# Performance work log

Measured on AMD Instinct MI355X. Metric: run time of the kernel, lower is better.

Reference implementation:

```python
import jax, jax.numpy as jnp
import numpy as np

N, L = 32, 2048
C_S, C_E, C_H, K, NRES = 384, 32, 128, 7, 20
C_IN = C_S + C_E  # 416
EPS = 1e-8


def setup_inputs() -> dict:
    key = jax.random.key(0)
    ks = jax.random.split(key, 32)
    s = 0.02
    d = {}
    d['aa_seq'] = jax.random.randint(ks[0], (L,), 0, NRES)
    d['sfea_tns'] = jax.random.normal(ks[1], (N, L, C_S), jnp.float32)
    d['sfea_tns_init'] = jax.random.normal(ks[2], (N, L, C_S), jnp.float32)
    d['encd_tns'] = jax.random.normal(ks[3], (N, L, C_E), jnp.float32)
    d['quat_tns'] = jax.random.normal(ks[4], (N, L, 4), jnp.float32)
    d['trsl_tns'] = jax.random.normal(ks[5], (N, L, 3), jnp.float32)
    # FrameHead linears
    d['Wq'] = jax.random.normal(ks[6], (C_IN, 4), jnp.float32) * s
    d['bq'] = jnp.zeros((4,), jnp.float32)
    d['Wt'] = jax.random.normal(ks[7], (C_IN, 3), jnp.float32) * s
    d['bt'] = jnp.zeros((3,), jnp.float32)
    # 20 per-residue-type AngleHead experts, stacked on leading axis
    d['Wa1'] = jax.random.normal(ks[8], (NRES, C_IN, C_H), jnp.float32) * s
    d['ba1'] = jnp.zeros((NRES, C_H), jnp.float32)
    d['Wa2'] = jax.random.normal(ks[9], (NRES, C_IN, C_H), jnp.float32) * s
    d['ba2'] = jnp.zeros((NRES, C_H), jnp.float32)
    d['Wb1a'] = jax.random.normal(ks[10], (NRES, C_H, C_H), jnp.float32) * s
    d['bb1a'] = jnp.zeros((NRES, C_H), jnp.float32)
    d['Wb1b'] = jax.random.normal(ks[11], (NRES, C_H, C_H), jnp.float32) * s
    d['bb1b'] = jnp.zeros((NRES, C_H), jnp.float32)
    d['Wb2a'] = jax.random.normal(ks[12], (NRES, C_H, C_H), jnp.float32) * s
    d['bb2a'] = jnp.zeros((NRES, C_H), jnp.float32)
    d['Wb2b'] = jax.random.normal(ks[13], (NRES, C_H, C_H), jnp.float32) * s
    d['bb2b'] = jnp.zeros((NRES, C_H), jnp.float32)
    d['Wout'] = jax.random.normal(ks[14], (NRES, C_H, K * 2), jnp.float32) * s
    d['bout'] = jnp.zeros((NRES, K * 2), jnp.float32)
    return d


def _qnorm(q):
    return q * jax.lax.rsqrt(jnp.sum(q * q, -1, keepdims=True) + EPS)


def _quat_mul(q, p):
    w1, x1, y1, z1 = jnp.split(q, 4, -1)
    w2, x2, y2, z2 = jnp.split(p, 4, -1)
    return jnp.concatenate([
        w1 * w2 - x1 * x2 - y1 * y2 - z1 * z2,
        w1 * x2 + x1 * w2 + y1 * z2 - z1 * y2,
        w1 * y2 - x1 * z2 + y1 * w2 + z1 * x2,
        w1 * z2 + x1 * y2 - y1 * x2 + z1 * w2], -1)


def _quat_rotate(q, v):
    # rotate vector v by unit quaternion q = (w, xyz)
    w, qv = q[..., :1], q[..., 1:]
    t = 2.0 * jnp.cross(qv, v)
    return v + w * t + jnp.cross(qv, t)


def _angle_net(sfcd, sfcd_init, aa, Wa1, ba1, Wa2, ba2,
               Wb1a, bb1a, Wb1b, bb1b, Wb2a, bb2a, Wb2b, bb2b, Wout, bout):
    # residue-type routed AngleHead: gather each token's expert weights by aa index
    g = lambda W: jnp.take(W, aa, axis=0)  # [L, ...]
    relu = jax.nn.relu
    a = (jnp.einsum('nlc,lch->nlh', relu(sfcd), g(Wa1)) + g(ba1)
         + jnp.einsum('nlc,lch->nlh', relu(sfcd_init), g(Wa2)) + g(ba2))
    # residual block 1
    h = jnp.einsum('nlh,lhk->nlk', relu(a), g(Wb1a)) + g(bb1a)
    a = a + jnp.einsum('nlh,lhk->nlk', relu(h), g(Wb1b)) + g(bb1b)
    # residual block 2
    h = jnp.einsum('nlh,lhk->nlk', relu(a), g(Wb2a)) + g(bb2a)
    a = a + jnp.einsum('nlh,lhk->nlk', relu(h), g(Wb2b)) + g(bb2b)
    out = jnp.einsum('nlh,lhk->nlk', relu(a), g(Wout)) + g(bout)  # [N,L,2K]
    ang = out.reshape(out.shape[0], out.shape[1], K, 2)
    norm = jnp.sqrt(jnp.sum(ang * ang, -1, keepdims=True) + 1e-12)
    return ang / norm


def reference(aa_seq, sfea_tns, sfea_tns_init, encd_tns, quat_tns, trsl_tns,
              Wq, bq, Wt, bt, Wa1, ba1, Wa2, ba2, Wb1a, bb1a, Wb1b, bb1b,
              Wb2a, bb2a, Wb2b, bb2b, Wout, bout):
    sfcd = jnp.concatenate([sfea_tns, encd_tns], -1)          # [N,L,C_IN]
    sfcd_init = jnp.concatenate([sfea_tns_init, encd_tns], -1)
    # FrameHead: quaternion/translation update signals
    quat_upd = sfcd @ Wq + bq                                  # [N,L,4]
    trsl_upd = sfcd @ Wt + bt                                  # [N,L,3]
    q_old = _qnorm(quat_tns)
    quat_new = _qnorm(_quat_mul(q_old, _qnorm(quat_upd)))
    trsl_new = trsl_tns + _quat_rotate(q_old, trsl_upd)
    angl_tns = _angle_net(sfcd, sfcd_init, aa_seq, Wa1, ba1, Wa2, ba2,
                          Wb1a, bb1a, Wb1b, bb1b, Wb2a, bb2a, Wb2b, bb2b,
                          Wout, bout)
    return quat_new, trsl_new, angl_tns, quat_upd
```

## Files before the change

kernel.cpp:

```cpp
#include <hip/hip_runtime.h>

#define L_SEQ 2048
#define CS 384
#define CE 32
#define CIN 416
#define CH 128
#define NRES 20

#define ABST 136
#define PADN 2068
#define NB2  1034

#define PERM_REGION 4608
#define WA_PER (CH*CIN)
#define WB_PER (CH*CH)
#define WO_PER (16*CH)
#define OFF_WA1T 0
#define OFF_WA2T (NRES*WA_PER)
#define OFF_WB1AT (2*NRES*WA_PER)
#define OFF_WB1BT (OFF_WB1AT + 1*NRES*WB_PER)
#define OFF_WB2AT (OFF_WB1AT + 2*NRES*WB_PER)
#define OFF_WB2BT (OFF_WB1AT + 3*NRES*WB_PER)
#define OFF_WOUTT (OFF_WB1AT + 4*NRES*WB_PER)
#define TOTW (OFF_WOUTT + NRES*WO_PER)

#define OUT_TR 262144
#define OUT_ANG 458752
#define OUT_QU 1376256

#define LOSCALE 4096.0f
#define ILOSCALE (1.0f/4096.0f)
#define F16MIN 6.1035156e-5f

typedef _Float16 f16x8 __attribute__((ext_vector_type(8)));
typedef _Float16 f16x4 __attribute__((ext_vector_type(4)));
typedef float f32x4 __attribute__((ext_vector_type(4)));

#define MFMA16 __builtin_amdgcn_mfma_f32_16x16x32_f16

static __device__ __forceinline__ void split1(float x, _Float16& h, _Float16& l) {
  _Float16 hi = (__builtin_fabsf(x) < F16MIN) ? (_Float16)0.f : (_Float16)x;
  h = hi;
  l = (_Float16)((x - (float)hi) * LOSCALE);
}

__global__ __launch_bounds__(256) void quat_head(
    const float* __restrict__ sfea, const float* __restrict__ encd,
    const float* __restrict__ quat, const float* __restrict__ trsl,
    const float* __restrict__ Wq, const float* __restrict__ bq,
    const float* __restrict__ Wt, const float* __restrict__ bt,
    float* __restrict__ out) {
  const int wv   = threadIdx.x >> 6;
  const int lane = threadIdx.x & 63;
  const size_t idx = (size_t)blockIdx.x * 4 + wv;
  const float* __restrict__ srow = sfea + idx * CS;

  float q0=0,q1=0,q2=0,q3=0,t0=0,t1=0,t2=0;
  #pragma unroll
  for (int cc = 0; cc < 6; ++cc) {
    const int ch = cc*64 + lane;
    const float s = srow[ch];
    const float4 wq = *reinterpret_cast<const float4*>(Wq + (size_t)ch*4);
    const float* wt = Wt + (size_t)ch*3;
    q0 += s*wq.x; q1 += s*wq.y; q2 += s*wq.z; q3 += s*wq.w;
    t0 += s*wt[0]; t1 += s*wt[1]; t2 += s*wt[2];
  }
  if (lane < CE) {
    const float s = encd[idx*CE + lane];
    const int ch = CS + lane;
    const float4 wq = *reinterpret_cast<const float4*>(Wq + (size_t)ch*4);
    const float* wt = Wt + (size_t)ch*3;
    q0 += s*wq.x; q1 += s*wq.y; q2 += s*wq.z; q3 += s*wq.w;
    t0 += s*wt[0]; t1 += s*wt[1]; t2 += s*wt[2];
  }
  #pragma unroll
  for (int off = 1; off < 64; off <<= 1) {
    q0 += __shfl_xor(q0, off); q1 += __shfl_xor(q1, off);
    q2 += __shfl_xor(q2, off); q3 += __shfl_xor(q3, off);
    t0 += __shfl_xor(t0, off); t1 += __shfl_xor(t1, off);
    t2 += __shfl_xor(t2, off);
  }
  if (lane == 0) {
    const float u0 = q0 + bq[0], u1 = q1 + bq[1], u2 = q2 + bq[2], u3 = q3 + bq[3];
    const float v0 = t0 + bt[0], v1 = t1 + bt[1], v2 = t2 + bt[2];
    float a0 = quat[idx*4+0], a1 = quat[idx*4+1], a2 = quat[idx*4+2], a3 = quat[idx*4+3];
    const float rq = rsqrtf(a0*a0+a1*a1+a2*a2+a3*a3 + 1e-8f);
    a0*=rq; a1*=rq; a2*=rq; a3*=rq;
    const float ru = rsqrtf(u0*u0+u1*u1+u2*u2+u3*u3 + 1e-8f);
    const float p0=u0*ru, p1=u1*ru, p2=u2*ru, p3=u3*ru;
    const float mw = a0*p0 - a1*p1 - a2*p2 - a3*p3;
    const float mx = a0*p1 + a1*p0 + a2*p3 - a3*p2;
    const float my = a0*p2 - a1*p3 + a2*p0 + a3*p1;
    const float mz = a0*p3 + a1*p2 - a2*p1 + a3*p0;
    const float rm = rsqrtf(mw*mw+mx*mx+my*my+mz*mz + 1e-8f);
    out[idx*4+0]=mw*rm; out[idx*4+1]=mx*rm; out[idx*4+2]=my*rm; out[idx*4+3]=mz*rm;
    const float tx = 2.f*(a2*v2 - a3*v1);
    const float ty = 2.f*(a3*v0 - a1*v2);
    const float tz = 2.f*(a1*v1 - a2*v0);
    out[OUT_TR + idx*3+0] = trsl[idx*3+0] + v0 + a0*tx + (a2*tz - a3*ty);
    out[OUT_TR + idx*3+1] = trsl[idx*3+1] + v1 + a0*ty + (a3*tx - a1*tz);
    out[OUT_TR + idx*3+2] = trsl[idx*3+2] + v2 + a0*tz + (a1*ty - a2*tx);
    out[OUT_QU + idx*4+0]=u0; out[OUT_QU + idx*4+1]=u1;
    out[OUT_QU + idx*4+2]=u2; out[OUT_QU + idx*4+3]=u3;
  }
}

__global__ __launch_bounds__(1024) void build_perm(const int* __restrict__ aa_seq,
                                                   unsigned short* __restrict__ perm) {
  __shared__ int cnt[NRES*32];
  __shared__ int woff[NRES*32];
  __shared__ int poff_s[NRES];
  __shared__ int ctot_s[NRES];
  const int t = threadIdx.x;
  const int wv = t >> 6, lane = t & 63;

  for (int i = t; i < PADN; i += 1024) perm[i] = 0;

  int aav[2];
  #pragma unroll
  for (int h = 0; h < 2; ++h) {
    const int W = wv + h*16;
    aav[h] = aa_seq[W*64 + lane];
    #pragma unroll
    for (int a = 0; a < NRES; ++a) {
      const unsigned long long m = __ballot(aav[h] == a);
      if (lane == a) cnt[a*32 + W] = (int)__popcll(m);
    }
  }
  __syncthreads();
  if (t < 32) {
    int tot = 0;
    if (t < NRES) {
      #pragma unroll
      for (int W = 0; W < 32; ++W) tot += cnt[t*32 + W];
    }
    const int pa = (t < NRES) ? ((tot + 1) & ~1) : 0;
    int s = pa;
    #pragma unroll
    for (int o = 1; o < 32; o <<= 1) {
      const int u = __shfl_up(s, o);
      if (lane >= o) s += u;
    }
    if (t < NRES) { poff_s[t] = s - pa; ctot_s[t] = tot; }
    for (int a = 0; a < NRES; ++a) {
      const int v0 = cnt[a*32 + t];
      int v = v0;
      #pragma unroll
      for (int o = 1; o < 32; o <<= 1) {
        const int u = __shfl_up(v, o);
        if (lane >= o) v += u;
      }
      woff[a*32 + t] = poff_s[a] + v - v0;
    }
  }
  __syncthreads();
  const unsigned long long ltmask = (lane == 0) ? 0ull : (~0ull >> (64 - lane));
  #pragma unroll
  for (int h = 0; h < 2; ++h) {
    const int W = wv + h*16;
    const int a = aav[h];
    int pos = 0;
    #pragma unroll
    for (int aq = 0; aq < NRES; ++aq) {
      const unsigned long long m = __ballot(a == aq);
      if (a == aq) pos = woff[aq*32 + W] + (int)__popcll(m & ltmask);
    }
    const unsigned short lv = (unsigned short)(W*64 + lane);
    perm[pos] = lv;
    if ((ctot_s[a] & 1) && pos == poff_s[a] + ctot_s[a] - 1) perm[pos + 1] = lv;
  }
}

__global__ __launch_bounds__(256) void convert_w(
    const float* __restrict__ Wa1, const float* __restrict__ Wa2,
    const float* __restrict__ Wb1a, const float* __restrict__ Wb1b,
    const float* __restrict__ Wb2a, const float* __restrict__ Wb2b,
    const float* __restrict__ Wout, _Float16* __restrict__ wsw) {
  const int idx = blockIdx.x * 256 + threadIdx.x;
  if (idx >= TOTW) return;
  float v;
  if (idx < OFF_WB1AT) {
    const int which = (idx < OFF_WA2T) ? 0 : 1;
    const float* W = which ? Wa2 : Wa1;
    int r = idx - which * OFF_WA2T;
    const int aa = r / WA_PER; r -= aa * WA_PER;
    const int h = r / CIN;     const int c = r - h * CIN;
    v = W[((size_t)aa*CIN + c)*CH + h];
  } else if (idx < OFF_WOUTT) {
    int q = idx - OFF_WB1AT;
    const int which = q / (NRES*WB_PER);
    int r = q - which * (NRES*WB_PER);
    const float* W = (which==0)?Wb1a:(which==1)?Wb1b:(which==2)?Wb2a:Wb2b;
    const int aa = r / WB_PER; r -= aa * WB_PER;
    const int h = r / CH;      const int c = r - h * CH;
    v = W[((size_t)aa*CH + c)*CH + h];
  } else {
    int r = idx - OFF_WOUTT;
    const int aa = r / WO_PER; r -= aa * WO_PER;
    const int kk = r / CH;     const int c = r - kk * CH;
    v = (kk < 14) ? Wout[((size_t)aa*CH + c)*14 + kk] : 0.f;
  }
  _Float16 h, l; split1(v, h, l);
  wsw[idx] = h;
  wsw[(size_t)TOTW + idx] = l;
}

static __device__ __forceinline__ void fold(f32x4 acc[2][2], const f32x4 accL[2][2],
                                            float b0, float b1) {
  #pragma unroll
  for (int m = 0; m < 2; ++m)
    #pragma unroll
    for (int i = 0; i < 4; ++i) {
      acc[m][0][i] += accL[m][0][i]*ILOSCALE + b0;
      acc[m][1][i] += accL[m][1][i]*ILOSCALE + b1;
    }
}

static __device__ __forceinline__ void store_relu_pair(_Float16* dh, _Float16* dl,
    const f32x4 acc[2][2], int lane, int h0) {
  const int lr = lane & 15;
  const int r0 = (lane >> 4) << 2;
  #pragma unroll
  for (int m = 0; m < 2; ++m)
    #pragma unroll
    for (int p = 0; p < 2; ++p)
      #pragma unroll
      for (int i = 0; i < 4; ++i) {
        const float v = fmaxf(acc[m][p][i], 0.f);
        _Float16 hh, ll; split1(v, hh, ll);
        const int idx = (m*16 + r0 + i)*ABST + h0 + p*16 + lr;
        dh[idx] = hh; dl[idx] = ll;
      }
}

template<int S>
static __device__ __forceinline__ void gemm_dual(
    const _Float16* aH0, const _Float16* aL0,
    const _Float16* aH1, const _Float16* aL1,
    const _Float16* __restrict__ wH,
    int kbase, int nks,
    f32x4 acc0[2][2], f32x4 acc0L[2][2],
    f32x4 acc1[2][2], f32x4 acc1L[2][2],
    int lane, int h0) {
  const int lr = lane & 15;
  const int lk = (lane >> 4) << 3;
  #pragma unroll
  for (int ks = 0; ks < nks; ++ks) {
    const int kl = ks*32 + lk;
    const int kg = kbase + kl;
    const _Float16* p0 = wH + (size_t)(h0+lr)*S + kg;
    const _Float16* p1 = wH + (size_t)(h0+16+lr)*S + kg;
    const f16x8 b0h = *(const f16x8*)p0;
    const f16x8 b0l = *(const f16x8*)(p0 + TOTW);
    const f16x8 b1h = *(const f16x8*)p1;
    const f16x8 b1l = *(const f16x8*)(p1 + TOTW);
#define DOPOS(AH, AL, AC, ACL) { \
    const f16x8 a0h = *(const f16x8*)(AH + lr*ABST + kl); \
    const f16x8 a0l = *(const f16x8*)(AL + lr*ABST + kl); \
    const f16x8 a1h = *(const f16x8*)(AH + (lr+16)*ABST + kl); \
    const f16x8 a1l = *(const f16x8*)(AL + (lr+16)*ABST + kl); \
    AC[0][0]  = MFMA16(a0h, b0h, AC[0][0], 0,0,0); \
    ACL[0][0] = MFMA16(a0h, b0l, ACL[0][0], 0,0,0); \
    ACL[0][0] = MFMA16(a0l, b0h, ACL[0][0], 0,0,0); \
    AC[1][0]  = MFMA16(a1h, b0h, AC[1][0], 0,0,0); \
    ACL[1][0] = MFMA16(a1h, b0l, ACL[1][0], 0,0,0); \
    ACL[1][0] = MFMA16(a1l, b0h, ACL[1][0], 0,0,0); \
    AC[0][1]  = MFMA16(a0h, b1h, AC[0][1], 0,0,0); \
    ACL[0][1] = MFMA16(a0h, b1l, ACL[0][1], 0,0,0); \
    ACL[0][1] = MFMA16(a0l, b1h, ACL[0][1], 0,0,0); \
    AC[1][1]  = MFMA16(a1h, b1h, AC[1][1], 0,0,0); \
    ACL[1][1] = MFMA16(a1h, b1l, ACL[1][1], 0,0,0); \
    ACL[1][1] = MFMA16(a1l, b1h, ACL[1][1], 0,0,0); }
    DOPOS(aH0, aL0, acc0, acc0L)
    DOPOS(aH1, aL1, acc1, acc1L)
#undef DOPOS
  }
}

static __device__ __forceinline__ void stage_row128(
    const float* __restrict__ row, _Float16* dH, _Float16* dL, int n, int sj) {
  #pragma unroll
  for (int q2 = 0; q2 < 2; ++q2) {
    const int cl = q2*64 + sj*8;
    const float4 v0 = *(const float4*)(row + cl);
    const float4 v1 = *(const float4*)(row + cl + 4);
    const float xs[8] = {v0.x,v0.y,v0.z,v0.w,v1.x,v1.y,v1.z,v1.w};
    f16x8 h8, l8;
    #pragma unroll
    for (int e = 0; e < 8; ++e) {
      _Float16 hh, ll; split1(fmaxf(xs[e], 0.f), hh, ll);
      h8[e] = hh; l8[e] = ll;
    }
    *(f16x8*)(dH + n*ABST + cl) = h8;
    *(f16x8*)(dL + n*ABST + cl) = l8;
  }
}

static __device__ __forceinline__ void stage_encd(
    const float* __restrict__ erow,
    _Float16* sH, _Float16* sL, _Float16* iH, _Float16* iL, int n, int sj) {
  const int cl = sj*4;
  const float4 v = *(const float4*)(erow + cl);
  const float xs[4] = {v.x, v.y, v.z, v.w};
  f16x4 h4, l4;
  #pragma unroll
  for (int e = 0; e < 4; ++e) {
    _Float16 hh, ll; split1(fmaxf(xs[e], 0.f), hh, ll);
    h4[e] = hh; l4[e] = ll;
  }
  *(f16x4*)(sH + n*ABST + cl) = h4;  *(f16x4*)(sL + n*ABST + cl) = l4;
  *(f16x4*)(iH + n*ABST + cl) = h4;  *(f16x4*)(iL + n*ABST + cl) = l4;
}

__global__ __launch_bounds__(256, 2) void fah_main(
    const int* __restrict__ aa_seq, const unsigned short* __restrict__ perm,
    const float* __restrict__ sfea, const float* __restrict__ sfei,
    const float* __restrict__ encd,
    const float* __restrict__ ba1, const float* __restrict__ ba2,
    const float* __restrict__ bb1a, const float* __restrict__ bb1b,
    const float* __restrict__ bb2a, const float* __restrict__ bb2b,
    const float* __restrict__ bout,
    const _Float16* __restrict__ wsw,
    float* __restrict__ out) {
  __shared__ __align__(16) _Float16 sf0H[32*ABST], sf0L[32*ABST];
  __shared__ __align__(16) _Float16 in0H[32*ABST], in0L[32*ABST];
  __shared__ __align__(16) _Float16 sf1H[32*ABST], sf1L[32*ABST];
  __shared__ __align__(16) _Float16 in1H[32*ABST], in1L[32*ABST];
  _Float16 *ab0H = sf0H, *ab0L = sf0L, *hb0H = in0H, *hb0L = in0L;
  _Float16 *ab1H = sf1H, *ab1L = sf1L, *hb1H = in1H, *hb1L = in1L;

  const int orig = blockIdx.x;
  const int xcd = orig & 7, i8 = orig >> 3;
  const int sp = (xcd < 2 ? xcd*130 : 260 + (xcd-2)*129) + i8;
  const int l0 = perm[2*sp], l1 = perm[2*sp+1];
  const int aa = aa_seq[l0];

  const int t = threadIdx.x;
  const int lane = t & 63, wv = t >> 6;
  const int lr = lane & 15, lk = (lane >> 4) << 3, h0 = wv * 32;
  const int n = t >> 3, sj = t & 7;

  const f32x4 zz = {0.f, 0.f, 0.f, 0.f};
  f32x4 accA0[2][2], accA0L[2][2], accA1[2][2], accA1L[2][2];
  #pragma unroll
  for (int m = 0; m < 2; ++m) {
    accA0[m][0]=zz; accA0[m][1]=zz; accA0L[m][0]=zz; accA0L[m][1]=zz;
    accA1[m][0]=zz; accA1[m][1]=zz; accA1L[m][0]=zz; accA1L[m][1]=zz;
  }

  const _Float16* wsA1 = wsw + OFF_WA1T + (size_t)aa*WA_PER;
  const _Float16* wsA2 = wsw + OFF_WA2T + (size_t)aa*WA_PER;

  #pragma unroll
  for (int ck = 0; ck < 4; ++ck) {
    const int koff = ck * 128;
    if (ck < 3) {
      stage_row128(sfea + ((size_t)n*L_SEQ + l0)*CS + koff, sf0H, sf0L, n, sj);
      stage_row128(sfei + ((size_t)n*L_SEQ + l0)*CS + koff, in0H, in0L, n, sj);
      stage_row128(sfea + ((size_t)n*L_SEQ + l1)*CS + koff, sf1H, sf1L, n, sj);
      stage_row128(sfei + ((size_t)n*L_SEQ + l1)*CS + koff, in1H, in1L, n, sj);
    } else {
      stage_encd(encd + ((size_t)n*L_SEQ + l0)*CE, sf0H, sf0L, in0H, in0L, n, sj);
      stage_encd(encd + ((size_t)n*L_SEQ + l1)*CE, sf1H, sf1L, in1H, in1L, n, sj);
    }
    __syncthreads();
    const int nks = (ck < 3) ? 4 : 1;
    gemm_dual<CIN>(sf0H, sf0L, sf1H, sf1L, wsA1, koff, nks,
                   accA0, accA0L, accA1, accA1L, lane, h0);
    gemm_dual<CIN>(in0H, in0L, in1H, in1L, wsA2, koff, nks,
                   accA0, accA0L, accA1, accA1L, lane, h0);
    __syncthreads();
  }

  {
    const float b0v = ba1[aa*CH + h0 + lr]      + ba2[aa*CH + h0 + lr];
    const float b1v = ba1[aa*CH + h0 + 16 + lr] + ba2[aa*CH + h0 + 16 + lr];
    fold(accA0, accA0L, b0v, b1v);
    fold(accA1, accA1L, b0v, b1v);
    store_relu_pair(ab0H, ab0L, accA0, lane, h0);
    store_relu_pair(ab1H, ab1L, accA1, lane, h0);
  }
  __syncthreads();

  {
    f32x4 c0[2][2], c0L[2][2], c1[2][2], c1L[2][2];
    #pragma unroll
    for (int m = 0; m < 2; ++m) { c0[m][0]=zz;c0[m][1]=zz;c0L[m][0]=zz;c0L[m][1]=zz;
                                  c1[m][0]=zz;c1[m][1]=zz;c1L[m][0]=zz;c1L[m][1]=zz; }
    gemm_dual<CH>(ab0H, ab0L, ab1H, ab1L, wsw + OFF_WB1AT + (size_t)aa*WB_PER, 0, 4,
                  c0, c0L, c1, c1L, lane, h0);
    const float B0 = bb1a[aa*CH + h0 + lr], B1 = bb1a[aa*CH + h0 + 16 + lr];
    fold(c0, c0L, B0, B1); fold(c1, c1L, B0, B1);
    store_relu_pair(hb0H, hb0L, c0, lane, h0);
    store_relu_pair(hb1H, hb1L, c1, lane, h0);
  }
  __syncthreads();
  {
    f32x4 c0L[2][2], c1L[2][2];
    #pragma unroll
    for (int m = 0; m < 2; ++m) { c0L[m][0]=zz;c0L[m][1]=zz;c1L[m][0]=zz;c1L[m][1]=zz; }
    gemm_dual<CH>(hb0H, hb0L, hb1H, hb1L, wsw + OFF_WB1BT + (size_t)aa*WB_PER, 0, 4,
                  accA0, c0L, accA1, c1L, lane, h0);
    const float B0 = bb1b[aa*CH + h0 + lr], B1 = bb1b[aa*CH + h0 + 16 + lr];
    fold(accA0, c0L, B0, B1); fold(accA1, c1L, B0, B1);
    store_relu_pair(ab0H, ab0L, accA0, lane, h0);
    store_relu_pair(ab1H, ab1L, accA1, lane, h0);
  }
  __syncthreads();
  {
    f32x4 c0[2][2], c0L[2][2], c1[2][2], c1L[2][2];
    #pragma unroll
    for (int m = 0; m < 2; ++m) { c0[m][0]=zz;c0[m][1]=zz;c0L[m][0]=zz;c0L[m][1]=zz;
                                  c1[m][0]=zz;c1[m][1]=zz;c1L[m][0]=zz;c1L[m][1]=zz; }
    gemm_dual<CH>(ab0H, ab0L, ab1H, ab1L, wsw + OFF_WB2AT + (size_t)aa*WB_PER, 0, 4,
                  c0, c0L, c1, c1L, lane, h0);
    const float B0 = bb2a[aa*CH + h0 + lr], B1 = bb2a[aa*CH + h0 + 16 + lr];
    fold(c0, c0L, B0, B1); fold(c1, c1L, B0, B1);
    store_relu_pair(hb0H, hb0L, c0, lane, h0);
    store_relu_pair(hb1H, hb1L, c1, lane, h0);
  }
  __syncthreads();
  {
    f32x4 c0L[2][2], c1L[2][2];
    #pragma unroll
    for (int m = 0; m < 2; ++m) { c0L[m][0]=zz;c0L[m][1]=zz;c1L[m][0]=zz;c1L[m][1]=zz; }
    gemm_dual<CH>(hb0H, hb0L, hb1H, hb1L, wsw + OFF_WB2BT + (size_t)aa*WB_PER, 0, 4,
                  accA0, c0L, accA1, c1L, lane, h0);
    const float B0 = bb2b[aa*CH + h0 + lr], B1 = bb2b[aa*CH + h0 + 16 + lr];
    fold(accA0, c0L, B0, B1); fold(accA1, c1L, B0, B1);
    store_relu_pair(ab0H, ab0L, accA0, lane, h0);
    store_relu_pair(ab1H, ab1L, accA1, lane, h0);
  }
  __syncthreads();

  {
    const int pos  = wv >> 1;
    const int half = wv & 1;
    const _Float16* aH = pos ? ab1H : ab0H;
    const _Float16* aL = pos ? ab1L : ab0L;
    const int lsel = pos ? l1 : l0;
    f32x4 o = zz, oL = zz;
    #pragma unroll
    for (int ks = 0; ks < 4; ++ks) {
      const int k = ks*32 + lk;
      const f16x8 ah = *(const f16x8*)(aH + (half*16 + lr)*ABST + k);
      const f16x8 al = *(const f16x8*)(aL + (half*16 + lr)*ABST + k);
      const _Float16* p = wsw + OFF_WOUTT + (size_t)aa*WO_PER + (size_t)lr*CH + k;
      const f16x8 bh = *(const f16x8*)p;
      const f16x8 bl = *(const f16x8*)(p + TOTW);
      o  = MFMA16(ah, bh, o,  0,0,0);
      oL = MFMA16(ah, bl, oL, 0,0,0);
      oL = MFMA16(al, bh, oL, 0,0,0);
    }
    const float bo = (lr < 14) ? bout[aa*14 + lr] : 0.f;
    #pragma unroll
    for (int i = 0; i < 4; ++i) {
      const float v  = o[i] + oL[i]*ILOSCALE + bo;
      const float pv = __shfl_xor(v, 1);
      const float r  = rsqrtf(v*v + pv*pv + 1e-12f);
      if (lr < 14) {
        const int nrow = half*16 + ((lane >> 4) << 2) + i;
        out[OUT_ANG + (size_t)nrow*(L_SEQ*14) + (size_t)lsel*14 + lr] = v*r;
      }
    }
  }
}

extern "C" void kernel_launch(void* const* d_in, const int* in_sizes, int n_in,
                              void* d_out, int out_size, void* d_ws, size_t ws_size,
                              hipStream_t stream) {
  const int*   aa   = (const int*)  d_in[0];
  const float* sfea = (const float*)d_in[1];
  const float* sfei = (const float*)d_in[2];
  const float* encd = (const float*)d_in[3];
  const float* quat = (const float*)d_in[4];
  const float* trsl = (const float*)d_in[5];
  const float* Wq   = (const float*)d_in[6];
  const float* bq   = (const float*)d_in[7];
  const float* Wt   = (const float*)d_in[8];
  const float* bt   = (const float*)d_in[9];
  const float* Wa1  = (const float*)d_in[10];
  const float* ba1  = (const float*)d_in[11];
  const float* Wa2  = (const float*)d_in[12];
  const float* ba2  = (const float*)d_in[13];
  const float* Wb1a = (const float*)d_in[14];
  const float* bb1a = (const float*)d_in[15];
  const float* Wb1b = (const float*)d_in[16];
  const float* bb1b = (const float*)d_in[17];
  const float* Wb2a = (const float*)d_in[18];
  const float* bb2a = (const float*)d_in[19];
  const float* Wb2b = (const float*)d_in[20];
  const float* bb2b = (const float*)d_in[21];
  const float* Wout = (const float*)d_in[22];
  const float* bout = (const float*)d_in[23];
  float* out = (float*)d_out;

  unsigned short* perm = (unsigned short*)d_ws;
  _Float16* wsw = (_Float16*)((char*)d_ws + PERM_REGION);

  hipLaunchKernelGGL(build_perm, dim3(1), dim3(1024), 0, stream, aa, perm);
  hipLaunchKernelGGL(convert_w, dim3((TOTW + 255)/256), dim3(256), 0, stream,
                     Wa1, Wa2, Wb1a, Wb1b, Wb2a, Wb2b, Wout, wsw);
  hipLaunchKernelGGL(quat_head, dim3(16384), dim3(256), 0, stream,
                     sfea, encd, quat, trsl, Wq, bq, Wt, bt, out);
  hipLaunchKernelGGL(fah_main, dim3(NB2), dim3(256), 0, stream,
                     aa, perm, sfea, sfei, encd,
                     ba1, ba2, bb1a, bb1b, bb2a, bb2b, bout, wsw, out);
}
```

Measured before the change: 209.2 us.

## Split fah_main into 512 threads with one wave group per sequence position

Doubles the fah_main block to 512 threads: waves 0-3 handle position l0 and waves 4-7 handle position l1, each computing one position's GEMM tiles instead of both. Staging is redistributed over more threads, with fewer elements per thread. This halves per-thread accumulator registers and MFMA work per wave, aiming for more latency hiding. The costs are that each weight fragment is now loaded by two waves instead of one, and barriers now span more waves.

```diff
diff --git a/kernel.cpp b/kernel.cpp
--- a/kernel.cpp
+++ b/kernel.cpp
@@ -34,6 +34,7 @@
 
 typedef _Float16 f16x8 __attribute__((ext_vector_type(8)));
 typedef _Float16 f16x4 __attribute__((ext_vector_type(4)));
+typedef _Float16 f16x2 __attribute__((ext_vector_type(2)));
 typedef float f32x4 __attribute__((ext_vector_type(4)));
 
 #define MFMA16 __builtin_amdgcn_mfma_f32_16x16x32_f16
@@ -234,13 +235,11 @@
 }
 
 template<int S>
-static __device__ __forceinline__ void gemm_dual(
-    const _Float16* aH0, const _Float16* aL0,
-    const _Float16* aH1, const _Float16* aL1,
+static __device__ __forceinline__ void gemm_p(
+    const _Float16* aH, const _Float16* aL,
     const _Float16* __restrict__ wH,
     int kbase, int nks,
-    f32x4 acc0[2][2], f32x4 acc0L[2][2],
-    f32x4 acc1[2][2], f32x4 acc1L[2][2],
+    f32x4 acc[2][2], f32x4 accL[2][2],
     int lane, int h0) {
   const int lr = lane & 15;
   const int lk = (lane >> 4) << 3;
@@ -254,65 +253,55 @@
     const f16x8 b0l = *(const f16x8*)(p0 + TOTW);
     const f16x8 b1h = *(const f16x8*)p1;
     const f16x8 b1l = *(const f16x8*)(p1 + TOTW);
-#define DOPOS(AH, AL, AC, ACL) { \
-    const f16x8 a0h = *(const f16x8*)(AH + lr*ABST + kl); \
-    const f16x8 a0l = *(const f16x8*)(AL + lr*ABST + kl); \
-    const f16x8 a1h = *(const f16x8*)(AH + (lr+16)*ABST + kl); \
-    const f16x8 a1l = *(const f16x8*)(AL + (lr+16)*ABST + kl); \
-    AC[0][0]  = MFMA16(a0h, b0h, AC[0][0], 0,0,0); \
-    ACL[0][0] = MFMA16(a0h, b0l, ACL[0][0], 0,0,0); \
-    ACL[0][0] = MFMA16(a0l, b0h, ACL[0][0], 0,0,0); \
-    AC[1][0]  = MFMA16(a1h, b0h, AC[1][0], 0,0,0); \
-    ACL[1][0] = MFMA16(a1h, b0l, ACL[1][0], 0,0,0); \
-    ACL[1][0] = MFMA16(a1l, b0h, ACL[1][0], 0,0,0); \
-    AC[0][1]  = MFMA16(a0h, b1h, AC[0][1], 0,0,0); \
-    ACL[0][1] = MFMA16(a0h, b1l, ACL[0][1], 0,0,0); \
-    ACL[0][1] = MFMA16(a0l, b1h, ACL[0][1], 0,0,0); \
-    AC[1][1]  = MFMA16(a1h, b1h, AC[1][1], 0,0,0); \
-    ACL[1][1] = MFMA16(a1h, b1l, ACL[1][1], 0,0,0); \
-    ACL[1][1] = MFMA16(a1l, b1h, ACL[1][1], 0,0,0); }
-    DOPOS(aH0, aL0, acc0, acc0L)
-    DOPOS(aH1, aL1, acc1, acc1L)
-#undef DOPOS
+    const f16x8 a0h = *(const f16x8*)(aH + lr*ABST + kl);
+    const f16x8 a0l = *(const f16x8*)(aL + lr*ABST + kl);
+    const f16x8 a1h = *(const f16x8*)(aH + (lr+16)*ABST + kl);
+    const f16x8 a1l = *(const f16x8*)(aL + (lr+16)*ABST + kl);
+    acc [0][0] = MFMA16(a0h, b0h, acc [0][0], 0,0,0);
+    accL[0][0] = MFMA16(a0h, b0l, accL[0][0], 0,0,0);
+    accL[0][0] = MFMA16(a0l, b0h, accL[0][0], 0,0,0);
+    acc [1][0] = MFMA16(a1h, b0h, acc [1][0], 0,0,0);
+    accL[1][0] = MFMA16(a1h, b0l, accL[1][0], 0,0,0);
+    accL[1][0] = MFMA16(a1l, b0h, accL[1][0], 0,0,0);
+    acc [0][1] = MFMA16(a0h, b1h, acc [0][1], 0,0,0);
+    accL[0][1] = MFMA16(a0h, b1l, accL[0][1], 0,0,0);
+    accL[0][1] = MFMA16(a0l, b1h, accL[0][1], 0,0,0);
+    acc [1][1] = MFMA16(a1h, b1h, acc [1][1], 0,0,0);
+    accL[1][1] = MFMA16(a1h, b1l, accL[1][1], 0,0,0);
+    accL[1][1] = MFMA16(a1l, b1h, accL[1][1], 0,0,0);
   }
 }
 
 static __device__ __forceinline__ void stage_row128(
     const float* __restrict__ row, _Float16* dH, _Float16* dL, int n, int sj) {
-  #pragma unroll
-  for (int q2 = 0; q2 < 2; ++q2) {
-    const int cl = q2*64 + sj*8;
-    const float4 v0 = *(const float4*)(row + cl);
-    const float4 v1 = *(const float4*)(row + cl + 4);
-    const float xs[8] = {v0.x,v0.y,v0.z,v0.w,v1.x,v1.y,v1.z,v1.w};
-    f16x8 h8, l8;
-    #pragma unroll
-    for (int e = 0; e < 8; ++e) {
-      _Float16 hh, ll; split1(fmaxf(xs[e], 0.f), hh, ll);
-      h8[e] = hh; l8[e] = ll;
-    }
-    *(f16x8*)(dH + n*ABST + cl) = h8;
-    *(f16x8*)(dL + n*ABST + cl) = l8;
-  }
+  const int cl = sj*8;
+  const float4 v0 = *(const float4*)(row + cl);
+  const float4 v1 = *(const float4*)(row + cl + 4);
+  const float xs[8] = {v0.x,v0.y,v0.z,v0.w,v1.x,v1.y,v1.z,v1.w};
+  f16x8 h8, l8;
+  #pragma unroll
+  for (int e = 0; e < 8; ++e) {
+    _Float16 hh, ll; split1(fmaxf(xs[e], 0.f), hh, ll);
+    h8[e] = hh; l8[e] = ll;
+  }
+  *(f16x8*)(dH + n*ABST + cl) = h8;
+  *(f16x8*)(dL + n*ABST + cl) = l8;
 }
 
 static __device__ __forceinline__ void stage_encd(
     const float* __restrict__ erow,
     _Float16* sH, _Float16* sL, _Float16* iH, _Float16* iL, int n, int sj) {
-  const int cl = sj*4;
-  const float4 v = *(const float4*)(erow + cl);
-  const float xs[4] = {v.x, v.y, v.z, v.w};
-  f16x4 h4, l4;
-  #pragma unroll
-  for (int e = 0; e < 4; ++e) {
-    _Float16 hh, ll; split1(fmaxf(xs[e], 0.f), hh, ll);
-    h4[e] = hh; l4[e] = ll;
-  }
-  *(f16x4*)(sH + n*ABST + cl) = h4;  *(f16x4*)(sL + n*ABST + cl) = l4;
-  *(f16x4*)(iH + n*ABST + cl) = h4;  *(f16x4*)(iL + n*ABST + cl) = l4;
-}
-
-__global__ __launch_bounds__(256, 2) void fah_main(
+  const int cl = sj*2;
+  const float2 v = *(const float2*)(erow + cl);
+  _Float16 h0v, l0v, h1v, l1v;
+  split1(fmaxf(v.x, 0.f), h0v, l0v);
+  split1(fmaxf(v.y, 0.f), h1v, l1v);
+  f16x2 h2, l2; h2[0]=h0v; h2[1]=h1v; l2[0]=l0v; l2[1]=l1v;
+  *(f16x2*)(sH + n*ABST + cl) = h2;  *(f16x2*)(sL + n*ABST + cl) = l2;
+  *(f16x2*)(iH + n*ABST + cl) = h2;  *(f16x2*)(iL + n*ABST + cl) = l2;
+}
+
+__global__ __launch_bounds__(512, 2) void fah_main(
     const int* __restrict__ aa_seq, const unsigned short* __restrict__ perm,
     const float* __restrict__ sfea, const float* __restrict__ sfei,
     const float* __restrict__ encd,
@@ -337,16 +326,24 @@
 
   const int t = threadIdx.x;
   const int lane = t & 63, wv = t >> 6;
-  const int lr = lane & 15, lk = (lane >> 4) << 3, h0 = wv * 32;
-  const int n = t >> 3, sj = t & 7;
+  const int lr = lane & 15, lk = (lane >> 4) << 3;
+  const int pos = wv >> 2;
+  const int h0  = (wv & 3) * 32;
+  const int n = t >> 4, sj = t & 15;
+
+  const _Float16* mysfH = pos ? sf1H : sf0H;
+  const _Float16* mysfL = pos ? sf1L : sf0L;
+  const _Float16* myinH = pos ? in1H : in0H;
+  const _Float16* myinL = pos ? in1L : in0L;
+  _Float16* myabH = pos ? ab1H : ab0H;
+  _Float16* myabL = pos ? ab1L : ab0L;
+  _Float16* myhbH = pos ? hb1H : hb0H;
+  _Float16* myhbL = pos ? hb1L : hb0L;
 
   const f32x4 zz = {0.f, 0.f, 0.f, 0.f};
-  f32x4 accA0[2][2], accA0L[2][2], accA1[2][2], accA1L[2][2];
-  #pragma unroll
-  for (int m = 0; m < 2; ++m) {
-    accA0[m][0]=zz; accA0[m][1]=zz; accA0L[m][0]=zz; accA0L[m][1]=zz;
-    accA1[m][0]=zz; accA1[m][1]=zz; accA1L[m][0]=zz; accA1L[m][1]=zz;
-  }
+  f32x4 accA[2][2], accAL[2][2];
+  #pragma unroll
+  for (int m = 0; m < 2; ++m) { accA[m][0]=zz; accA[m][1]=zz; accAL[m][0]=zz; accAL[m][1]=zz; }
 
   const _Float16* wsA1 = wsw + OFF_WA1T + (size_t)aa*WA_PER;
   const _Float16* wsA2 = wsw + OFF_WA2T + (size_t)aa*WA_PER;
@@ -365,80 +362,62 @@
     }
     __syncthreads();
     const int nks = (ck < 3) ? 4 : 1;
-    gemm_dual<CIN>(sf0H, sf0L, sf1H, sf1L, wsA1, koff, nks,
-                   accA0, accA0L, accA1, accA1L, lane, h0);
-    gemm_dual<CIN>(in0H, in0L, in1H, in1L, wsA2, koff, nks,
-                   accA0, accA0L, accA1, accA1L, lane, h0);
+    gemm_p<CIN>(mysfH, mysfL, wsA1, koff, nks, accA, accAL, lane, h0);
+    gemm_p<CIN>(myinH, myinL, wsA2, koff, nks, accA, accAL, lane, h0);
     __syncthreads();
   }
 
   {
     const float b0v = ba1[aa*CH + h0 + lr]      + ba2[aa*CH + h0 + lr];
     const float b1v = ba1[aa*CH + h0 + 16 + lr] + ba2[aa*CH + h0 + 16 + lr];
-    fold(accA0, accA0L, b0v, b1v);
-    fold(accA1, accA1L, b0v, b1v);
-    store_relu_pair(ab0H, ab0L, accA0, lane, h0);
-    store_relu_pair(ab1H, ab1L, accA1, lane, h0);
+    fold(accA, accAL, b0v, b1v);
+    store_relu_pair(myabH, myabL, accA, lane, h0);
   }
   __syncthreads();
 
   {
-    f32x4 c0[2][2], c0L[2][2], c1[2][2], c1L[2][2];
-    #pragma unroll
-    for (int m = 0; m < 2; ++m) { c0[m][0]=zz;c0[m][1]=zz;c0L[m][0]=zz;c0L[m][1]=zz;
-                                  c1[m][0]=zz;c1[m][1]=zz;c1L[m][0]=zz;c1L[m][1]=zz; }
-    gemm_dual<CH>(ab0H, ab0L, ab1H, ab1L, wsw + OFF_WB1AT + (size_t)aa*WB_PER, 0, 4,
-                  c0, c0L, c1, c1L, lane, h0);
-    const float B0 = bb1a[aa*CH + h0 + lr], B1 = bb1a[aa*CH + h0 + 16 + lr];
-    fold(c0, c0L, B0, B1); fold(c1, c1L, B0, B1);
-    store_relu_pair(hb0H, hb0L, c0, lane, h0);
-    store_relu_pair(hb1H, hb1L, c1, lane, h0);
+    f32x4 c[2][2], cL[2][2];
+    #pragma unroll
+    for (int m = 0; m < 2; ++m) { c[m][0]=zz; c[m][1]=zz; cL[m][0]=zz; cL[m][1]=zz; }
+    gemm_p<CH>(myabH, myabL, wsw + OFF_WB1AT + (size_t)aa*WB_PER, 0, 4, c, cL, lane, h0);
+    fold(c, cL, bb1a[aa*CH + h0 + lr], bb1a[aa*CH + h0 + 16 + lr]);
+    store_relu_pair(myhbH, myhbL, c, lane, h0);
   }
   __syncthreads();
   {
-    f32x4 c0L[2][2], c1L[2][2];
-    #pragma unroll
-    for (int m = 0; m < 2; ++m) { c0L[m][0]=zz;c0L[m][1]=zz;c1L[m][0]=zz;c1L[m][1]=zz; }
-    gemm_dual<CH>(hb0H, hb0L, hb1H, hb1L, wsw + OFF_WB1BT + (size_t)aa*WB_PER, 0, 4,
-                  accA0, c0L, accA1, c1L, lane, h0);
-    const float B0 = bb1b[aa*CH + h0 + lr], B1 = bb1b[aa*CH + h0 + 16 + lr];
-    fold(accA0, c0L, B0, B1); fold(accA1, c1L, B0, B1);
-    store_relu_pair(ab0H, ab0L, accA0, lane, h0);
-    store_relu_pair(ab1H, ab1L, accA1, lane, h0);
+    f32x4 cL[2][2];
+    #pragma unroll
+    for (int m = 0; m < 2; ++m) { cL[m][0]=zz; cL[m][1]=zz; }
+    gemm_p<CH>(myhbH, myhbL, wsw + OFF_WB1BT + (size_t)aa*WB_PER, 0, 4, accA, cL, lane, h0);
+    fold(accA, cL, bb1b[aa*CH + h0 + lr], bb1b[aa*CH + h0 + 16 + lr]);
+    store_relu_pair(myabH, myabL, accA, lane, h0);
   }
   __syncthreads();
   {
-    f32x4 c0[2][2], c0L[2][2], c1[2][2], c1L[2][2];
-    #pragma unroll
-    for (int m = 0; m < 2; ++m) { c0[m][0]=zz;c0[m][1]=zz;c0L[m][0]=zz;c0L[m][1]=zz;
-                                  c1[m][0]=zz;c1[m][1]=zz;c1L[m][0]=zz;c1L[m][1]=zz; }
-    gemm_dual<CH>(ab0H, ab0L, ab1H, ab1L, wsw + OFF_WB2AT + (size_t)aa*WB_PER, 0, 4,
-                  c0, c0L, c1, c1L, lane, h0);
-    const float B0 = bb2a[aa*CH + h0 + lr], B1 = bb2a[aa*CH + h0 + 16 + lr];
-    fold(c0, c0L, B0, B1); fold(c1, c1L, B0, B1);
-    store_relu_pair(hb0H, hb0L, c0, lane, h0);
-    store_relu_pair(hb1H, hb1L, c1, lane, h0);
+    f32x4 c[2][2], cL[2][2];
+    #pragma unroll
+    for (int m = 0; m < 2; ++m) { c[m][0]=zz; c[m][1]=zz; cL[m][0]=zz; cL[m][1]=zz; }
+    gemm_p<CH>(myabH, myabL, wsw + OFF_WB2AT + (size_t)aa*WB_PER, 0, 4, c, cL, lane, h0);
+    fold(c, cL, bb2a[aa*CH + h0 + lr], bb2a[aa*CH + h0 + 16 + lr]);
+    store_relu_pair(myhbH, myhbL, c, lane, h0);
   }
   __syncthreads();
   {
-    f32x4 c0L[2][2], c1L[2][2];
-    #pragma unroll
-    for (int m = 0; m < 2; ++m) { c0L[m][0]=zz;c0L[m][1]=zz;c1L[m][0]=zz;c1L[m][1]=zz; }
-    gemm_dual<CH>(hb0H, hb0L, hb1H, hb1L, wsw + OFF_WB2BT + (size_t)aa*WB_PER, 0, 4,
-                  accA0, c0L, accA1, c1L, lane, h0);
-    const float B0 = bb2b[aa*CH + h0 + lr], B1 = bb2b[aa*CH + h0 + 16 + lr];
-    fold(accA0, c0L, B0, B1); fold(accA1, c1L, B0, B1);
-    store_relu_pair(ab0H, ab0L, accA0, lane, h0);
-    store_relu_pair(ab1H, ab1L, accA1, lane, h0);
-  }
-  __syncthreads();
-
-  {
-    const int pos  = wv >> 1;
+    f32x4 cL[2][2];
+    #pragma unroll
+    for (int m = 0; m < 2; ++m) { cL[m][0]=zz; cL[m][1]=zz; }
+    gemm_p<CH>(myhbH, myhbL, wsw + OFF_WB2BT + (size_t)aa*WB_PER, 0, 4, accA, cL, lane, h0);
+    fold(accA, cL, bb2b[aa*CH + h0 + lr], bb2b[aa*CH + h0 + 16 + lr]);
+    store_relu_pair(myabH, myabL, accA, lane, h0);
+  }
+  __syncthreads();
+
+  if (wv < 4) {
+    const int opos = wv >> 1;
     const int half = wv & 1;
-    const _Float16* aH = pos ? ab1H : ab0H;
-    const _Float16* aL = pos ? ab1L : ab0L;
-    const int lsel = pos ? l1 : l0;
+    const _Float16* aH = opos ? ab1H : ab0H;
+    const _Float16* aL = opos ? ab1L : ab0L;
+    const int lsel = opos ? l1 : l0;
     f32x4 o = zz, oL = zz;
     #pragma unroll
     for (int ks = 0; ks < 4; ++ks) {
@@ -503,7 +482,7 @@
                      Wa1, Wa2, Wb1a, Wb1b, Wb2a, Wb2b, Wout, wsw);
   hipLaunchKernelGGL(quat_head, dim3(16384), dim3(256), 0, stream,
                      sfea, encd, quat, trsl, Wq, bq, Wt, bt, out);
-  hipLaunchKernelGGL(fah_main, dim3(NB2), dim3(256), 0, stream,
+  hipLaunchKernelGGL(fah_main, dim3(NB2), dim3(512), 0, stream,
                      aa, perm, sfea, sfei, encd,
                      ba1, ba2, bb1a, bb1b, bb2a, bb2b, bout, wsw, out);
 }
```

New measurement: 251.7 us. +20.3%, slower.

## Software-pipeline weight and activation loads across GEMM stages into registers

Applied to the files above, without the earlier changes.

Restructures the angle-net kernel so that weight fragments for the next K-chunk or next layer are loaded into registers while the current chunk's MFMAs run. The sfea_init rows for the next chunk are prefetched into registers before they are staged to LDS. __syncthreads is replaced by an LDS-only waitcnt plus s_barrier, so outstanding global loads are no longer drained at each barrier. This hides global-memory latency behind compute, at the cost of many more live registers (B fragment arrays plus prefetch buffers), which risks spills or lower occupancy under launch_bounds(256,2).

```diff
diff --git a/kernel.cpp b/kernel.cpp
--- a/kernel.cpp
+++ b/kernel.cpp
@@ -37,6 +37,8 @@
 typedef float f32x4 __attribute__((ext_vector_type(4)));
 
 #define MFMA16 __builtin_amdgcn_mfma_f32_16x16x32_f16
+
+#define BAR() { asm volatile("s_waitcnt lgkmcnt(0)" ::: "memory"); __builtin_amdgcn_s_barrier(); }
 
 static __device__ __forceinline__ void split1(float x, _Float16& h, _Float16& l) {
   _Float16 hi = (__builtin_fabsf(x) < F16MIN) ? (_Float16)0.f : (_Float16)x;
@@ -233,27 +235,35 @@
       }
 }
 
-template<int S>
-static __device__ __forceinline__ void gemm_dual(
+template<int S, int NKS>
+static __device__ __forceinline__ void loadB(const _Float16* __restrict__ wH,
+    int kbase, int lane, int h0, f16x8 (&B)[NKS][4]) {
+  const int lr = lane & 15, lk = (lane >> 4) << 3;
+  #pragma unroll
+  for (int ks = 0; ks < NKS; ++ks) {
+    const int kg = kbase + ks*32 + lk;
+    const _Float16* p0 = wH + (size_t)(h0+lr)*S + kg;
+    const _Float16* p1 = wH + (size_t)(h0+16+lr)*S + kg;
+    B[ks][0] = *(const f16x8*)p0;
+    B[ks][1] = *(const f16x8*)(p0 + TOTW);
+    B[ks][2] = *(const f16x8*)p1;
+    B[ks][3] = *(const f16x8*)(p1 + TOTW);
+  }
+}
+
+template<int NKS>
+static __device__ __forceinline__ void computeDual(
     const _Float16* aH0, const _Float16* aL0,
     const _Float16* aH1, const _Float16* aL1,
-    const _Float16* __restrict__ wH,
-    int kbase, int nks,
+    const f16x8 (&B)[NKS][4],
     f32x4 acc0[2][2], f32x4 acc0L[2][2],
     f32x4 acc1[2][2], f32x4 acc1L[2][2],
-    int lane, int h0) {
-  const int lr = lane & 15;
-  const int lk = (lane >> 4) << 3;
-  #pragma unroll
-  for (int ks = 0; ks < nks; ++ks) {
+    int lane) {
+  const int lr = lane & 15, lk = (lane >> 4) << 3;
+  #pragma unroll
+  for (int ks = 0; ks < NKS; ++ks) {
     const int kl = ks*32 + lk;
-    const int kg = kbase + kl;
-    const _Float16* p0 = wH + (size_t)(h0+lr)*S + kg;
-    const _Float16* p1 = wH + (size_t)(h0+16+lr)*S + kg;
-    const f16x8 b0h = *(const f16x8*)p0;
-    const f16x8 b0l = *(const f16x8*)(p0 + TOTW);
-    const f16x8 b1h = *(const f16x8*)p1;
-    const f16x8 b1l = *(const f16x8*)(p1 + TOTW);
+    const f16x8 b0h = B[ks][0], b0l = B[ks][1], b1h = B[ks][2], b1l = B[ks][3];
 #define DOPOS(AH, AL, AC, ACL) { \
     const f16x8 a0h = *(const f16x8*)(AH + lr*ABST + kl); \
     const f16x8 a0l = *(const f16x8*)(AL + lr*ABST + kl); \
@@ -277,26 +287,45 @@
   }
 }
 
-static __device__ __forceinline__ void stage_row128(
+static __device__ __forceinline__ void wr8(const float4& v0, const float4& v1,
+    _Float16* dH, _Float16* dL, int n, int cl) {
+  const float xs[8] = {v0.x,v0.y,v0.z,v0.w,v1.x,v1.y,v1.z,v1.w};
+  f16x8 h8, l8;
+  #pragma unroll
+  for (int e = 0; e < 8; ++e) {
+    _Float16 hh, ll; split1(fmaxf(xs[e], 0.f), hh, ll);
+    h8[e] = hh; l8[e] = ll;
+  }
+  *(f16x8*)(dH + n*ABST + cl) = h8;
+  *(f16x8*)(dL + n*ABST + cl) = l8;
+}
+
+static __device__ __forceinline__ void stage_row_inline(
     const float* __restrict__ row, _Float16* dH, _Float16* dL, int n, int sj) {
   #pragma unroll
   for (int q2 = 0; q2 < 2; ++q2) {
     const int cl = q2*64 + sj*8;
-    const float4 v0 = *(const float4*)(row + cl);
-    const float4 v1 = *(const float4*)(row + cl + 4);
-    const float xs[8] = {v0.x,v0.y,v0.z,v0.w,v1.x,v1.y,v1.z,v1.w};
-    f16x8 h8, l8;
-    #pragma unroll
-    for (int e = 0; e < 8; ++e) {
-      _Float16 hh, ll; split1(fmaxf(xs[e], 0.f), hh, ll);
-      h8[e] = hh; l8[e] = ll;
-    }
-    *(f16x8*)(dH + n*ABST + cl) = h8;
-    *(f16x8*)(dL + n*ABST + cl) = l8;
-  }
-}
-
-static __device__ __forceinline__ void stage_encd(
+    wr8(*(const float4*)(row + cl), *(const float4*)(row + cl + 4), dH, dL, n, cl);
+  }
+}
+
+static __device__ __forceinline__ void pref_sfei(
+    const float* __restrict__ r0, const float* __restrict__ r1, int sj, float4 st[8]) {
+  st[0] = *(const float4*)(r0 + sj*8);      st[1] = *(const float4*)(r0 + sj*8 + 4);
+  st[2] = *(const float4*)(r0 + 64 + sj*8); st[3] = *(const float4*)(r0 + 64 + sj*8 + 4);
+  st[4] = *(const float4*)(r1 + sj*8);      st[5] = *(const float4*)(r1 + sj*8 + 4);
+  st[6] = *(const float4*)(r1 + 64 + sj*8); st[7] = *(const float4*)(r1 + 64 + sj*8 + 4);
+}
+
+static __device__ __forceinline__ void wr_sfei(float4 st[8],
+    _Float16* i0H, _Float16* i0L, _Float16* i1H, _Float16* i1L, int n, int sj) {
+  wr8(st[0], st[1], i0H, i0L, n, sj*8);
+  wr8(st[2], st[3], i0H, i0L, n, 64 + sj*8);
+  wr8(st[4], st[5], i1H, i1L, n, sj*8);
+  wr8(st[6], st[7], i1H, i1L, n, 64 + sj*8);
+}
+
+static __device__ __forceinline__ void stage_encd2(
     const float* __restrict__ erow,
     _Float16* sH, _Float16* sL, _Float16* iH, _Float16* iL, int n, int sj) {
   const int cl = sj*4;
@@ -340,6 +369,14 @@
   const int lr = lane & 15, lk = (lane >> 4) << 3, h0 = wv * 32;
   const int n = t >> 3, sj = t & 7;
 
+  const float* sfeaL0 = sfea + ((size_t)n*L_SEQ + l0)*CS;
+  const float* sfeaL1 = sfea + ((size_t)n*L_SEQ + l1)*CS;
+  const float* sfeiL0 = sfei + ((size_t)n*L_SEQ + l0)*CS;
+  const float* sfeiL1 = sfei + ((size_t)n*L_SEQ + l1)*CS;
+
+  const _Float16* wsA1 = wsw + OFF_WA1T + (size_t)aa*WA_PER;
+  const _Float16* wsA2 = wsw + OFF_WA2T + (size_t)aa*WA_PER;
+
   const f32x4 zz = {0.f, 0.f, 0.f, 0.f};
   f32x4 accA0[2][2], accA0L[2][2], accA1[2][2], accA1L[2][2];
   #pragma unroll
@@ -348,30 +385,53 @@
     accA1[m][0]=zz; accA1[m][1]=zz; accA1L[m][0]=zz; accA1L[m][1]=zz;
   }
 
-  const _Float16* wsA1 = wsw + OFF_WA1T + (size_t)aa*WA_PER;
-  const _Float16* wsA2 = wsw + OFF_WA2T + (size_t)aa*WA_PER;
-
-  #pragma unroll
-  for (int ck = 0; ck < 4; ++ck) {
-    const int koff = ck * 128;
-    if (ck < 3) {
-      stage_row128(sfea + ((size_t)n*L_SEQ + l0)*CS + koff, sf0H, sf0L, n, sj);
-      stage_row128(sfei + ((size_t)n*L_SEQ + l0)*CS + koff, in0H, in0L, n, sj);
-      stage_row128(sfea + ((size_t)n*L_SEQ + l1)*CS + koff, sf1H, sf1L, n, sj);
-      stage_row128(sfei + ((size_t)n*L_SEQ + l1)*CS + koff, in1H, in1L, n, sj);
-    } else {
-      stage_encd(encd + ((size_t)n*L_SEQ + l0)*CE, sf0H, sf0L, in0H, in0L, n, sj);
-      stage_encd(encd + ((size_t)n*L_SEQ + l1)*CE, sf1H, sf1L, in1H, in1L, n, sj);
-    }
-    __syncthreads();
-    const int nks = (ck < 3) ? 4 : 1;
-    gemm_dual<CIN>(sf0H, sf0L, sf1H, sf1L, wsA1, koff, nks,
-                   accA0, accA0L, accA1, accA1L, lane, h0);
-    gemm_dual<CIN>(in0H, in0L, in1H, in1L, wsA2, koff, nks,
-                   accA0, accA0L, accA1, accA1L, lane, h0);
-    __syncthreads();
-  }
-
+  f16x8 Ba[4][4], Bb[4][4];
+  float4 stp[8];
+
+  loadB<CIN,4>(wsA1, 0, lane, h0, Ba);
+  loadB<CIN,4>(wsA2, 0, lane, h0, Bb);
+  stage_row_inline(sfeaL0, sf0H, sf0L, n, sj);
+  stage_row_inline(sfeiL0, in0H, in0L, n, sj);
+  stage_row_inline(sfeaL1, sf1H, sf1L, n, sj);
+  stage_row_inline(sfeiL1, in1H, in1L, n, sj);
+  pref_sfei(sfeiL0 + 128, sfeiL1 + 128, sj, stp);
+  BAR();
+
+  computeDual<4>(sf0H,sf0L,sf1H,sf1L, Ba, accA0,accA0L,accA1,accA1L, lane);
+  loadB<CIN,4>(wsA1, 128, lane, h0, Ba);
+  computeDual<4>(in0H,in0L,in1H,in1L, Bb, accA0,accA0L,accA1,accA1L, lane);
+  loadB<CIN,4>(wsA2, 128, lane, h0, Bb);
+  BAR();
+  wr_sfei(stp, in0H, in0L, in1H, in1L, n, sj);
+  stage_row_inline(sfeaL0 + 128, sf0H, sf0L, n, sj);
+  stage_row_inline(sfeaL1 + 128, sf1H, sf1L, n, sj);
+  pref_sfei(sfeiL0 + 256, sfeiL1 + 256, sj, stp);
+  BAR();
+
+  computeDual<4>(sf0H,sf0L,sf1H,sf1L, Ba, accA0,accA0L,accA1,accA1L, lane);
+  loadB<CIN,4>(wsA1, 256, lane, h0, Ba);
+  computeDual<4>(in0H,in0L,in1H,in1L, Bb, accA0,accA0L,accA1,accA1L, lane);
+  loadB<CIN,4>(wsA2, 256, lane, h0, Bb);
+  BAR();
+  wr_sfei(stp, in0H, in0L, in1H, in1L, n, sj);
+  stage_row_inline(sfeaL0 + 256, sf0H, sf0L, n, sj);
+  stage_row_inline(sfeaL1 + 256, sf1H, sf1L, n, sj);
+  BAR();
+
+  f16x8 B3a[1][4], B3b[1][4];
+  computeDual<4>(sf0H,sf0L,sf1H,sf1L, Ba, accA0,accA0L,accA1,accA1L, lane);
+  loadB<CH,4>(wsw + OFF_WB1AT + (size_t)aa*WB_PER, 0, lane, h0, Ba);
+  computeDual<4>(in0H,in0L,in1H,in1L, Bb, accA0,accA0L,accA1,accA1L, lane);
+  loadB<CH,4>(wsw + OFF_WB1BT + (size_t)aa*WB_PER, 0, lane, h0, Bb);
+  loadB<CIN,1>(wsA1, 384, lane, h0, B3a);
+  loadB<CIN,1>(wsA2, 384, lane, h0, B3b);
+  BAR();
+  stage_encd2(encd + ((size_t)n*L_SEQ + l0)*CE, sf0H, sf0L, in0H, in0L, n, sj);
+  stage_encd2(encd + ((size_t)n*L_SEQ + l1)*CE, sf1H, sf1L, in1H, in1L, n, sj);
+  BAR();
+
+  computeDual<1>(sf0H,sf0L,sf1H,sf1L, B3a, accA0,accA0L,accA1,accA1L, lane);
+  computeDual<1>(in0H,in0L,in1H,in1L, B3b, accA0,accA0L,accA1,accA1L, lane);
   {
     const float b0v = ba1[aa*CH + h0 + lr]      + ba2[aa*CH + h0 + lr];
     const float b1v = ba1[aa*CH + h0 + 16 + lr] + ba2[aa*CH + h0 + 16 + lr];
@@ -380,74 +440,93 @@
     store_relu_pair(ab0H, ab0L, accA0, lane, h0);
     store_relu_pair(ab1H, ab1L, accA1, lane, h0);
   }
-  __syncthreads();
+  BAR();
 
   {
     f32x4 c0[2][2], c0L[2][2], c1[2][2], c1L[2][2];
     #pragma unroll
     for (int m = 0; m < 2; ++m) { c0[m][0]=zz;c0[m][1]=zz;c0L[m][0]=zz;c0L[m][1]=zz;
                                   c1[m][0]=zz;c1[m][1]=zz;c1L[m][0]=zz;c1L[m][1]=zz; }
-    gemm_dual<CH>(ab0H, ab0L, ab1H, ab1L, wsw + OFF_WB1AT + (size_t)aa*WB_PER, 0, 4,
-                  c0, c0L, c1, c1L, lane, h0);
+    computeDual<4>(ab0H,ab0L,ab1H,ab1L, Ba, c0,c0L,c1,c1L, lane);
     const float B0 = bb1a[aa*CH + h0 + lr], B1 = bb1a[aa*CH + h0 + 16 + lr];
     fold(c0, c0L, B0, B1); fold(c1, c1L, B0, B1);
     store_relu_pair(hb0H, hb0L, c0, lane, h0);
     store_relu_pair(hb1H, hb1L, c1, lane, h0);
   }
-  __syncthreads();
+  loadB<CH,4>(wsw + OFF_WB2AT + (size_t)aa*WB_PER, 0, lane, h0, Ba);
+  BAR();
+
   {
     f32x4 c0L[2][2], c1L[2][2];
     #pragma unroll
     for (int m = 0; m < 2; ++m) { c0L[m][0]=zz;c0L[m][1]=zz;c1L[m][0]=zz;c1L[m][1]=zz; }
-    gemm_dual<CH>(hb0H, hb0L, hb1H, hb1L, wsw + OFF_WB1BT + (size_t)aa*WB_PER, 0, 4,
-                  accA0, c0L, accA1, c1L, lane, h0);
+    computeDual<4>(hb0H,hb0L,hb1H,hb1L, Bb, accA0,c0L,accA1,c1L, lane);
     const float B0 = bb1b[aa*CH + h0 + lr], B1 = bb1b[aa*CH + h0 + 16 + lr];
     fold(accA0, c0L, B0, B1); fold(accA1, c1L, B0, B1);
     store_relu_pair(ab0H, ab0L, accA0, lane, h0);
     store_relu_pair(ab1H, ab1L, accA1, lane, h0);
   }
-  __syncthreads();
+  loadB<CH,4>(wsw + OFF_WB2BT + (size_t)aa*WB_PER, 0, lane, h0, Bb);
+  BAR();
+
+  f16x8 Bo[4][2];
   {
     f32x4 c0[2][2], c0L[2][2], c1[2][2], c1L[2][2];
     #pragma unroll
     for (int m = 0; m < 2; ++m) { c0[m][0]=zz;c0[m][1]=zz;c0L[m][0]=zz;c0L[m][1]=zz;
                                   c1[m][0]=zz;c1[m][1]=zz;c1L[m][0]=zz;c1L[m][1]=zz; }
-    gemm_dual<CH>(ab0H, ab0L, ab1H, ab1L, wsw + OFF_WB2AT + (size_t)aa*WB_PER, 0, 4,
-                  c0, c0L, c1, c1L, lane, h0);
+    computeDual<4>(ab0H,ab0L,ab1H,ab1L, Ba, c0,c0L,c1,c1L, lane);
     const float B0 = bb2a[aa*CH + h0 + lr], B1 = bb2a[aa*CH + h0 + 16 + lr];
     fold(c0, c0L, B0, B1); fold(c1, c1L, B0, B1);
     store_relu_pair(hb0H, hb0L, c0, lane, h0);
     store_relu_pair(hb1H, hb1L, c1, lane, h0);
   }
-  __syncthreads();
+  if (wv < 2) {
+    #pragma unroll
+    for (int ks = 0; ks < 4; ++ks) {
+      const int k = ks*32 + lk;
+      const _Float16* p = wsw + OFF_WOUTT + (size_t)aa*WO_PER + (size_t)lr*CH + k;
+      Bo[ks][0] = *(const f16x8*)p;
+      Bo[ks][1] = *(const f16x8*)(p + TOTW);
+    }
+  }
+  BAR();
+
   {
     f32x4 c0L[2][2], c1L[2][2];
     #pragma unroll
     for (int m = 0; m < 2; ++m) { c0L[m][0]=zz;c0L[m][1]=zz;c1L[m][0]=zz;c1L[m][1]=zz; }
-    gemm_dual<CH>(hb0H, hb0L, hb1H, hb1L, wsw + OFF_WB2BT + (size_t)aa*WB_PER, 0, 4,
-                  accA0, c0L, accA1, c1L, lane, h0);
+    computeDual<4>(hb0H,hb0L,hb1H,hb1L, Bb, accA0,c0L,accA1,c1L, lane);
     const float B0 = bb2b[aa*CH + h0 + lr], B1 = bb2b[aa*CH + h0 + 16 + lr];
     fold(accA0, c0L, B0, B1); fold(accA1, c1L, B0, B1);
     store_relu_pair(ab0H, ab0L, accA0, lane, h0);
     store_relu_pair(ab1H, ab1L, accA1, lane, h0);
   }
-  __syncthreads();
-
+  BAR();
+
+  if (wv < 2) {
+    const int opos = wv >> 1;
+    (void)opos;
+  }
   {
-    const int pos  = wv >> 1;
+    const int opos = wv >> 1;
     const int half = wv & 1;
-    const _Float16* aH = pos ? ab1H : ab0H;
-    const _Float16* aL = pos ? ab1L : ab0L;
-    const int lsel = pos ? l1 : l0;
+    const _Float16* aH = opos ? ab1H : ab0H;
+    const _Float16* aL = opos ? ab1L : ab0L;
+    const int lsel = opos ? l1 : l0;
     f32x4 o = zz, oL = zz;
     #pragma unroll
     for (int ks = 0; ks < 4; ++ks) {
       const int k = ks*32 + lk;
       const f16x8 ah = *(const f16x8*)(aH + (half*16 + lr)*ABST + k);
       const f16x8 al = *(const f16x8*)(aL + (half*16 + lr)*ABST + k);
-      const _Float16* p = wsw + OFF_WOUTT + (size_t)aa*WO_PER + (size_t)lr*CH + k;
-      const f16x8 bh = *(const f16x8*)p;
-      const f16x8 bl = *(const f16x8*)(p + TOTW);
+      f16x8 bh, bl;
+      if (wv < 2) { bh = Bo[ks][0]; bl = Bo[ks][1]; }
+      else {
+        const _Float16* p = wsw + OFF_WOUTT + (size_t)aa*WO_PER + (size_t)lr*CH + k;
+        bh = *(const f16x8*)p;
+        bl = *(const f16x8*)(p + TOTW);
+      }
       o  = MFMA16(ah, bh, o,  0,0,0);
       oL = MFMA16(ah, bl, oL, 0,0,0);
       oL = MFMA16(al, bh, oL, 0,0,0);
```

New measurement: 245.3 us. 17.2% more time.
